# Optimization experiments

Hardware: AMD Instinct MI355X
Metric: run time of the kernel (lower is better)

The kernel has to match this reference:

```python
import jax, jax.numpy as jnp
import numpy as np

N = 100000
E = 1600000
F_IN = 512
HID = 8
HEADS = 8
NUM_CLASSES = 40
NEG_SLOPE = 0.2


def setup_inputs() -> dict:
    key = jax.random.key(0)
    ks = jax.random.split(key, 12)
    x = jax.random.normal(ks[0], (N, F_IN), dtype=jnp.float32)
    edge_index = jax.random.randint(ks[1], (2, E), 0, N, dtype=jnp.int64)
    s1 = 1.0 / np.sqrt(F_IN)
    s2 = 1.0 / np.sqrt(HID * HEADS)
    W1 = jax.random.normal(ks[2], (F_IN, HEADS * HID), dtype=jnp.float32) * s1
    a_src1 = jax.random.normal(ks[3], (HEADS, HID), dtype=jnp.float32) * s1
    a_dst1 = jax.random.normal(ks[4], (HEADS, HID), dtype=jnp.float32) * s1
    b1 = jnp.zeros((HEADS * HID,), dtype=jnp.float32)
    W2 = jax.random.normal(ks[5], (HEADS * HID, NUM_CLASSES), dtype=jnp.float32) * s2
    a_src2 = jax.random.normal(ks[6], (1, NUM_CLASSES), dtype=jnp.float32) * s2
    a_dst2 = jax.random.normal(ks[7], (1, NUM_CLASSES), dtype=jnp.float32) * s2
    b2 = jnp.zeros((NUM_CLASSES,), dtype=jnp.float32)
    return {"x": x, "edge_index": edge_index, "W1": W1, "a_src1": a_src1,
            "a_dst1": a_dst1, "b1": b1, "W2": W2, "a_src2": a_src2,
            "a_dst2": a_dst2, "b2": b2}


def _gat_conv(x, src, dst, W, a_src, a_dst, b, heads, out_ch):
    # linear projection, per-head: [N, heads, out_ch]
    h = (x @ W).reshape(N, heads, out_ch)
    # per-node attention logits [N, heads]
    al_s = jnp.einsum('nhf,hf->nh', h, a_src)
    al_d = jnp.einsum('nhf,hf->nh', h, a_dst)
    # per-edge raw scores [E', heads]
    e = jax.nn.leaky_relu(al_s[src] + al_d[dst], NEG_SLOPE)
    # segment softmax over edges sharing a destination node
    m = jax.lax.stop_gradient(jax.ops.segment_max(e, dst, num_segments=N))
    m = jnp.where(jnp.isfinite(m), m, 0.0)
    e = jnp.exp(e - m[dst])
    denom = jax.ops.segment_sum(e, dst, num_segments=N)
    alpha = e / denom[dst]  # [E', heads]
    # scatter-weighted aggregation of gathered source features
    out = jax.ops.segment_sum(alpha[:, :, None] * h[src], dst, num_segments=N)
    return out.reshape(N, heads * out_ch) + b


def reference(x, edge_index, W1, a_src1, a_dst1, b1, W2, a_src2, a_dst2, b2):
    # PyG GATConv default: add self-loops
    loops = jnp.arange(N, dtype=edge_index.dtype)
    src = jnp.concatenate([edge_index[0], loops])
    dst = jnp.concatenate([edge_index[1], loops])
    h = _gat_conv(x, src, dst, W1, a_src1, a_dst1, b1, HEADS, HID)
    h = jax.nn.elu(h)
    # dropout(p=0.6) is identity in eval mode
    out = _gat_conv(h, src, dst, W2, a_src2, a_dst2, b2, 1, NUM_CLASSES)
    return jax.nn.log_softmax(out, axis=1)
```

## Files before the change

### kernel.cpp

```cpp
#include <hip/hip_runtime.h>
#include <hip/hip_bf16.h>
#include <cstdint>
#include <cstddef>

#define N_NODES 100000
#define N_EDGES 1600000
#define E_TOT   (N_EDGES + N_NODES)
#define F_IN    512
#define HEADS   8
#define HID     8
#define F_H     64
#define NC      40
#define NEG     0.2f

#define BSH    8
#define NB     391
#define CHUNKH 8192
#define NBH    ((E_TOT + CHUNKH - 1) / CHUNKH)
#define CHUNKF 8192
#define NBF    ((E_TOT + CHUNKF - 1) / CHUNKF)
#define CAP    7168
#define GEMM_G ((N_NODES + 63) / 64)

typedef __attribute__((ext_vector_type(8))) __bf16 bf16x8;
typedef __attribute__((ext_vector_type(4))) float f32x4;
typedef __attribute__((ext_vector_type(8))) unsigned short u16x8;

__device__ __forceinline__ float bf2f(unsigned short u) {
  unsigned int w = ((unsigned int)u) << 16;
  return __builtin_bit_cast(float, w);
}
__device__ __forceinline__ unsigned short f2bf(float f) {
  __hip_bfloat16 b = __float2bfloat16(f);
  return __builtin_bit_cast(unsigned short, b);
}
__device__ __forceinline__ float lrexp(float v) {
  v = (v > 0.f) ? v : NEG * v;
  return __expf(v);
}

__device__ __forceinline__ bool detect_i64(const int* __restrict__ ei) {
  int lane = threadIdx.x & 63;
  int v = ei[2 * lane + 1];
  return __ballot(v != 0) == 0ull;
}

__device__ __forceinline__ int load_dst(const int* __restrict__ ei, bool f, int i) {
  if (i < N_EDGES) return f ? ei[2 * (N_EDGES + i)] : ei[N_EDGES + i];
  return i - N_EDGES;
}
__device__ __forceinline__ int load_src(const int* __restrict__ ei, bool f, int i) {
  if (i < N_EDGES) return f ? ei[2 * i] : ei[i];
  return i - N_EDGES;
}

__global__ __launch_bounds__(256) void k_hist_pack(
    const int* __restrict__ ei, const float* __restrict__ W1,
    uint4* __restrict__ w1f, int* __restrict__ bcnt) {
  __shared__ int h[NB];
  const int t = threadIdx.x;
  if (blockIdx.x < 16) {
    int tid = blockIdx.x * 256 + t;
    int lane = tid & 63;
    int tt = (tid >> 6) & 3;
    int s = tid >> 8;
    int k0 = s * 32 + ((lane >> 4) << 3);
    int col = tt * 16 + (lane & 15);
    u16x8 v;
#pragma unroll
    for (int i = 0; i < 8; ++i) v[i] = f2bf(W1[(size_t)(k0 + i) * F_H + col]);
    w1f[tid] = __builtin_bit_cast(uint4, v);
    return;
  }
  const int blk = blockIdx.x - 16;
  const bool f = detect_i64(ei);
  for (int i = t; i < NB; i += 256) h[i] = 0;
  __syncthreads();
  const int base = blk * CHUNKH;
#pragma unroll
  for (int j = 0; j < CHUNKH / 256; ++j) {
    int i = base + t + j * 256;
    if (i < E_TOT) atomicAdd(&h[load_dst(ei, f, i) >> BSH], 1);
  }
  __syncthreads();
  for (int i = t; i < NB; i += 256)
    if (h[i]) atomicAdd(&bcnt[i], h[i]);
}

__global__ __launch_bounds__(512) void k_bscan(const int* __restrict__ bcnt,
                                               int* __restrict__ bstart,
                                               int* __restrict__ bcur,
                                               int* __restrict__ rowstart) {
  __shared__ int sh[512];
  const int t = threadIdx.x;
  int v = (t < NB) ? bcnt[t] : 0;
  sh[t] = v;
  __syncthreads();
  for (int d = 1; d < 512; d <<= 1) {
    int u = (t >= d) ? sh[t - d] : 0;
    __syncthreads();
    sh[t] += u;
    __syncthreads();
  }
  if (t < NB) {
    int e = sh[t] - v;
    bstart[t] = e;
    bcur[t] = e;
  }
  if (t == 0) { bstart[NB] = E_TOT; rowstart[N_NODES] = E_TOT; }
}

__global__ __launch_bounds__(256) void k_bfill(const int* __restrict__ ei,
                                               int* __restrict__ bcur,
                                               unsigned int* __restrict__ inter) {
  __shared__ unsigned int ent[CHUNKF];
  __shared__ int h[NB], ofs[NB], cur[NB], gpos[NB];
  const int t = threadIdx.x;
  const int base = blockIdx.x * CHUNKF;
  const bool f = detect_i64(ei);
  for (int i = t; i < NB; i += 256) h[i] = 0;
  __syncthreads();
#pragma unroll
  for (int j = 0; j < CHUNKF / 256; ++j) {
    int i = base + t + j * 256;
    if (i < E_TOT) atomicAdd(&h[load_dst(ei, f, i) >> BSH], 1);
  }
  __syncthreads();
  if (t < 64) {
    int loc[7];
    int s = 0;
#pragma unroll
    for (int k = 0; k < 7; ++k) {
      int ix = t * 7 + k;
      int hv = (ix < NB) ? h[ix] : 0;
      loc[k] = s;
      s += hv;
    }
    int incl = s;
    for (int dd = 1; dd < 64; dd <<= 1) {
      int u = __shfl_up(incl, dd);
      if (t >= dd) incl += u;
    }
    int excl = incl - s;
#pragma unroll
    for (int k = 0; k < 7; ++k) {
      int ix = t * 7 + k;
      if (ix < NB) ofs[ix] = excl + loc[k];
    }
  }
  __syncthreads();
  for (int i = t; i < NB; i += 256) {
    cur[i] = ofs[i];
    gpos[i] = h[i] ? atomicAdd(&bcur[i], h[i]) : 0;
  }
  __syncthreads();
#pragma unroll
  for (int j = 0; j < CHUNKF / 256; ++j) {
    int i = base + t + j * 256;
    if (i < E_TOT) {
      int s = load_src(ei, f, i);
      int d = load_dst(ei, f, i);
      int p = atomicAdd(&cur[d >> BSH], 1);
      ent[p] = ((unsigned int)(d & 255) << 24) | (unsigned int)s;
    }
  }
  __syncthreads();
  const int wv = t >> 6, ln = t & 63;
  for (int b = wv; b < NB; b += 4) {
    int c = h[b];
    if (!c) continue;
    int g = gpos[b], o = ofs[b];
    for (int i = ln; i < c; i += 64) inter[g + i] = ent[o + i];
  }
}

__global__ __launch_bounds__(256) void k_gemm1s(
    const float* __restrict__ x, const uint4* __restrict__ w1f,
    const float* __restrict__ a_src, const float* __restrict__ a_dst,
    unsigned short* __restrict__ h1b, float* __restrict__ als,
    float* __restrict__ ald) {
  constexpr int PITCH = 68;
  __shared__ float xs[64 * PITCH];
  const int t = threadIdx.x;
  const int lane = t & 63;
  const int wv = t >> 6;
  const int rb = blockIdx.x * 64;
  const int srow = t >> 4;
  const int scol = t & 15;
  const int myrow = wv * 16 + (lane & 15);
  const int koff = (lane >> 4) << 3;

  f32x4 acc[4];
#pragma unroll
  for (int i = 0; i < 4; ++i) acc[i] = (f32x4){0.f, 0.f, 0.f, 0.f};

  for (int kc = 0; kc < F_IN; kc += 64) {
    __syncthreads();
#pragma unroll
    for (int j = 0; j < 4; ++j) {
      int r = srow + j * 16;
      int gr = rb + r;
      float4 v = make_float4(0.f, 0.f, 0.f, 0.f);
      if (gr < N_NODES)
        v = *reinterpret_cast<const float4*>(&x[(size_t)gr * F_IN + kc + scol * 4]);
      *reinterpret_cast<float4*>(&xs[r * PITCH + scol * 4]) = v;
    }
    __syncthreads();
#pragma unroll
    for (int s2 = 0; s2 < 2; ++s2) {
      const int sg = (kc >> 5) + s2;
      float4 a0 = *reinterpret_cast<const float4*>(&xs[myrow * PITCH + s2 * 32 + koff]);
      float4 a1 = *reinterpret_cast<const float4*>(&xs[myrow * PITCH + s2 * 32 + koff + 4]);
      uint4 b0 = w1f[(sg * 4 + 0) * 64 + lane];
      uint4 b1 = w1f[(sg * 4 + 1) * 64 + lane];
      uint4 b2 = w1f[(sg * 4 + 2) * 64 + lane];
      uint4 b3 = w1f[(sg * 4 + 3) * 64 + lane];
      bf16x8 af;
      af[0] = (__bf16)a0.x; af[1] = (__bf16)a0.y;
      af[2] = (__bf16)a0.z; af[3] = (__bf16)a0.w;
      af[4] = (__bf16)a1.x; af[5] = (__bf16)a1.y;
      af[6] = (__bf16)a1.z; af[7] = (__bf16)a1.w;
      acc[0] = __builtin_amdgcn_mfma_f32_16x16x32_bf16(af, __builtin_bit_cast(bf16x8, b0), acc[0], 0, 0, 0);
      acc[1] = __builtin_amdgcn_mfma_f32_16x16x32_bf16(af, __builtin_bit_cast(bf16x8, b1), acc[1], 0, 0, 0);
      acc[2] = __builtin_amdgcn_mfma_f32_16x16x32_bf16(af, __builtin_bit_cast(bf16x8, b2), acc[2], 0, 0, 0);
      acc[3] = __builtin_amdgcn_mfma_f32_16x16x32_bf16(af, __builtin_bit_cast(bf16x8, b3), acc[3], 0, 0, 0);
    }
  }

  const int r0 = rb + wv * 16 + ((lane >> 4) << 2);
  const int c = lane & 15;
#pragma unroll
  for (int tt = 0; tt < 4; ++tt) {
#pragma unroll
    for (int i = 0; i < 4; ++i) {
      int r = r0 + i;
      if (r < N_NODES) h1b[(size_t)r * F_H + tt * 16 + c] = f2bf(acc[tt][i]);
    }
  }

  float asw[4], adw[4];
#pragma unroll
  for (int tt = 0; tt < 4; ++tt) {
    asw[tt] = a_src[tt * 16 + c];
    adw[tt] = a_dst[tt * 16 + c];
  }
  float sp[4][4], dp[4][4];
#pragma unroll
  for (int tt = 0; tt < 4; ++tt)
#pragma unroll
    for (int i = 0; i < 4; ++i) {
      sp[tt][i] = acc[tt][i] * asw[tt];
      dp[tt][i] = acc[tt][i] * adw[tt];
    }
#pragma unroll
  for (int dd = 1; dd < 8; dd <<= 1)
#pragma unroll
    for (int tt = 0; tt < 4; ++tt)
#pragma unroll
      for (int i = 0; i < 4; ++i) {
        sp[tt][i] += __shfl_xor(sp[tt][i], dd);
        dp[tt][i] += __shfl_xor(dp[tt][i], dd);
      }
  if ((c & 7) == 0) {
    const int hb = c >> 3;
#pragma unroll
    for (int i = 0; i < 4; ++i) {
      int r = r0 + i;
      if (r < N_NODES) {
#pragma unroll
        for (int tt = 0; tt < 4; ++tt) {
          als[(size_t)r * HEADS + tt * 2 + hb] = sp[tt][i];
          ald[(size_t)r * HEADS + tt * 2 + hb] = dp[tt][i];
        }
      }
    }
  }
}

__global__ __launch_bounds__(256) void k_cfill(const unsigned int* __restrict__ inter,
                                               const int* __restrict__ bstart,
                                               int* __restrict__ rowstart,
                                               int* __restrict__ csrc) {
  __shared__ unsigned int out_l[CAP];
  __shared__ int cnt[256], sc[256], cur2[256];
  const int t = threadIdx.x;
  const int b = blockIdx.x;
  const int segStart = bstart[b];
  const int L = bstart[b + 1] - segStart;
  cnt[t] = 0;
  __syncthreads();
  for (int i = t; i < L; i += 256) atomicAdd(&cnt[inter[segStart + i] >> 24], 1);
  __syncthreads();
  sc[t] = cnt[t];
  __syncthreads();
  for (int d = 1; d < 256; d <<= 1) {
    int v = (t >= d) ? sc[t - d] : 0;
    __syncthreads();
    sc[t] += v;
    __syncthreads();
  }
  const int excl = sc[t] - cnt[t];
  cur2[t] = excl;
  const int node = (b << BSH) + t;
  if (node < N_NODES) rowstart[node] = segStart + excl;
  __syncthreads();
  if (L <= CAP) {
    for (int i = t; i < L; i += 256) {
      unsigned int e = inter[segStart + i];
      int p = atomicAdd(&cur2[e >> 24], 1);
      out_l[p] = e & 0xFFFFFFu;
    }
    __syncthreads();
    for (int i = t; i < L; i += 256) csrc[segStart + i] = (int)out_l[i];
  } else {
    for (int i = t; i < L; i += 256) {
      unsigned int e = inter[segStart + i];
      int p = atomicAdd(&cur2[e >> 24], 1);
      csrc[segStart + p] = (int)(e & 0xFFFFFFu);
    }
  }
}

__global__ __launch_bounds__(256) void k_agg1n(
    const int* __restrict__ rowstart, const int* __restrict__ csrc,
    const unsigned short* __restrict__ h1b, const float* __restrict__ als,
    const float* __restrict__ ald, const float* __restrict__ b1,
    unsigned short* __restrict__ hactb) {
  const int w = (int)((blockIdx.x * 256 + threadIdx.x) >> 6);
  const int lane = threadIdx.x & 63;
  const int grp = lane >> 3;
  const int l = lane & 7;
  const int n = w * 8 + grp;
  const bool live = (n < N_NODES);
  const int e0 = live ? rowstart[n] : 0;
  const int e1 = live ? rowstart[n + 1] : 0;
  const float aldv = live ? ald[(size_t)n * HEADS + l] : 0.f;

  float den = 0.f;
  float acc[8];
#pragma unroll
  for (int k = 0; k < 8; ++k) acc[k] = 0.f;

  int e = e0;
  for (; e + 4 <= e1; e += 4) {
    int4 sv = *reinterpret_cast<const int4*>(&csrc[e]);
    float a0 = als[(size_t)sv.x * HEADS + l];
    float a1 = als[(size_t)sv.y * HEADS + l];
    float a2 = als[(size_t)sv.z * HEADS + l];
    float a3 = als[(size_t)sv.w * HEADS + l];
    uint4 u0 = *reinterpret_cast<const uint4*>(&h1b[(size_t)sv.x * F_H + l * 8]);
    uint4 u1 = *reinterpret_cast<const uint4*>(&h1b[(size_t)sv.y * F_H + l * 8]);
    uint4 u2 = *reinterpret_cast<const uint4*>(&h1b[(size_t)sv.z * F_H + l * 8]);
    uint4 u3 = *reinterpret_cast<const uint4*>(&h1b[(size_t)sv.w * F_H + l * 8]);
    float p0 = lrexp(a0 + aldv), p1 = lrexp(a1 + aldv);
    float p2 = lrexp(a2 + aldv), p3 = lrexp(a3 + aldv);
    den += (p0 + p1) + (p2 + p3);
    const unsigned int* q0 = &u0.x;
    const unsigned int* q1 = &u1.x;
    const unsigned int* q2 = &u2.x;
    const unsigned int* q3 = &u3.x;
#pragma unroll
    for (int k = 0; k < 4; ++k) {
      acc[2 * k]     += p0 * bf2f((unsigned short)q0[k]) + p1 * bf2f((unsigned short)q1[k])
                      + p2 * bf2f((unsigned short)q2[k]) + p3 * bf2f((unsigned short)q3[k]);
      acc[2 * k + 1] += p0 * bf2f((unsigned short)(q0[k] >> 16)) + p1 * bf2f((unsigned short)(q1[k] >> 16))
                      + p2 * bf2f((unsigned short)(q2[k] >> 16)) + p3 * bf2f((unsigned short)(q3[k] >> 16));
    }
  }
  for (; e < e1; ++e) {
    int s = csrc[e];
    float a = als[(size_t)s * HEADS + l];
    uint4 u = *reinterpret_cast<const uint4*>(&h1b[(size_t)s * F_H + l * 8]);
    float p = lrexp(a + aldv);
    den += p;
    const unsigned int* q = &u.x;
#pragma unroll
    for (int k = 0; k < 4; ++k) {
      acc[2 * k]     += p * bf2f((unsigned short)q[k]);
      acc[2 * k + 1] += p * bf2f((unsigned short)(q[k] >> 16));
    }
  }

  if (live) {
    float inv = 1.f / den;
    uint4 outw;
    unsigned int* ow = &outw.x;
#pragma unroll
    for (int k = 0; k < 4; ++k) {
      float ox = acc[2 * k] * inv + b1[l * 8 + 2 * k];
      float oy = acc[2 * k + 1] * inv + b1[l * 8 + 2 * k + 1];
      ox = (ox > 0.f) ? ox : expm1f(ox);
      oy = (oy > 0.f) ? oy : expm1f(oy);
      ow[k] = ((unsigned int)f2bf(oy) << 16) | (unsigned int)f2bf(ox);
    }
    *reinterpret_cast<uint4*>(&hactb[(size_t)n * F_H + l * 8]) = outw;
  }
}

__global__ __launch_bounds__(256) void k_l2proj(
    const unsigned short* __restrict__ hactb, const float* __restrict__ W2,
    const float* __restrict__ a_src2, const float* __restrict__ a_dst2,
    unsigned short* __restrict__ h2b, float* __restrict__ als2,
    float* __restrict__ ald2) {
  __shared__ float hs[64 * 68];
  __shared__ float w2s[F_H * NC];
  const int t = threadIdx.x;
  const int nb = blockIdx.x * 64;
  {
    int r0 = t >> 3, c8 = t & 7;
#pragma unroll
    for (int i = 0; i < 2; ++i) {
      int r = r0 + i * 32;
      int gr = nb + r;
      u16x8 v = (u16x8)(0);
      if (gr < N_NODES)
        v = *reinterpret_cast<const u16x8*>(&hactb[(size_t)gr * F_H + c8 * 8]);
#pragma unroll
      for (int k = 0; k < 8; ++k) hs[r * 68 + c8 * 8 + k] = bf2f(v[k]);
    }
  }
  for (int i = t; i < F_H * NC; i += 256) w2s[i] = W2[i];
  __syncthreads();

  const int node = t >> 2, cg = t & 3;
  float acc[10];
#pragma unroll
  for (int c = 0; c < 10; ++c) acc[c] = 0.f;
  for (int k = 0; k < F_H; ++k) {
    float xv = hs[node * 68 + k];
#pragma unroll
    for (int c = 0; c < 10; ++c) acc[c] += xv * w2s[k * NC + cg * 10 + c];
  }
  const int gn = nb + node;
  float ps = 0.f, pd = 0.f;
#pragma unroll
  for (int c = 0; c < 10; ++c) {
    ps += acc[c] * a_src2[cg * 10 + c];
    pd += acc[c] * a_dst2[cg * 10 + c];
  }
  ps += __shfl_xor(ps, 1); ps += __shfl_xor(ps, 2);
  pd += __shfl_xor(pd, 1); pd += __shfl_xor(pd, 2);
  if (gn < N_NODES) {
#pragma unroll
    for (int c = 0; c < 10; ++c) h2b[(size_t)gn * NC + cg * 10 + c] = f2bf(acc[c]);
    if (cg == 0) { als2[gn] = ps; ald2[gn] = pd; }
  }
}

__global__ __launch_bounds__(256) void k_agg2n(
    const int* __restrict__ rowstart, const int* __restrict__ csrc,
    const unsigned short* __restrict__ h2b, const float* __restrict__ als2,
    const float* __restrict__ ald2, const float* __restrict__ b2,
    float* __restrict__ out) {
  const int w = (int)((blockIdx.x * 256 + threadIdx.x) >> 6);
  const int lane = threadIdx.x & 63;
  const int grp = lane >> 3;
  const int l = lane & 7;
  const int n = w * 8 + grp;
  const bool live = (n < N_NODES);
  const int e0 = live ? rowstart[n] : 0;
  const int e1 = live ? rowstart[n + 1] : 0;
  const float aldv = live ? ald2[n] : 0.f;
  const bool act = (l < 5);
  const int fo = act ? l * 8 : 0;

  float den = 0.f;
  float acc[8];
#pragma unroll
  for (int k = 0; k < 8; ++k) acc[k] = 0.f;

  int e = e0;
  for (; e + 4 <= e1; e += 4) {
    int4 sv = *reinterpret_cast<const int4*>(&csrc[e]);
    float a0 = als2[sv.x], a1 = als2[sv.y], a2 = als2[sv.z], a3 = als2[sv.w];
    uint4 u0 = *reinterpret_cast<const uint4*>(&h2b[(size_t)sv.x * NC + fo]);
    uint4 u1 = *reinterpret_cast<const uint4*>(&h2b[(size_t)sv.y * NC + fo]);
    uint4 u2 = *reinterpret_cast<const uint4*>(&h2b[(size_t)sv.z * NC + fo]);
    uint4 u3 = *reinterpret_cast<const uint4*>(&h2b[(size_t)sv.w * NC + fo]);
    float p0 = lrexp(a0 + aldv), p1 = lrexp(a1 + aldv);
    float p2 = lrexp(a2 + aldv), p3 = lrexp(a3 + aldv);
    den += (p0 + p1) + (p2 + p3);
    const unsigned int* q0 = &u0.x;
    const unsigned int* q1 = &u1.x;
    const unsigned int* q2 = &u2.x;
    const unsigned int* q3 = &u3.x;
#pragma unroll
    for (int k = 0; k < 4; ++k) {
      acc[2 * k]     += p0 * bf2f((unsigned short)q0[k]) + p1 * bf2f((unsigned short)q1[k])
                      + p2 * bf2f((unsigned short)q2[k]) + p3 * bf2f((unsigned short)q3[k]);
      acc[2 * k + 1] += p0 * bf2f((unsigned short)(q0[k] >> 16)) + p1 * bf2f((unsigned short)(q1[k] >> 16))
                      + p2 * bf2f((unsigned short)(q2[k] >> 16)) + p3 * bf2f((unsigned short)(q3[k] >> 16));
    }
  }
  for (; e < e1; ++e) {
    int s = csrc[e];
    float a = als2[s];
    uint4 u = *reinterpret_cast<const uint4*>(&h2b[(size_t)s * NC + fo]);
    float p = lrexp(a + aldv);
    den += p;
    const unsigned int* q = &u.x;
#pragma unroll
    for (int k = 0; k < 4; ++k) {
      acc[2 * k]     += p * bf2f((unsigned short)q[k]);
      acc[2 * k + 1] += p * bf2f((unsigned short)(q[k] >> 16));
    }
  }

  float o[8];
  float inv = 1.f / den;
  float mx = -1e30f;
#pragma unroll
  for (int k = 0; k < 8; ++k) {
    o[k] = act ? (acc[k] * inv + b2[fo + k]) : -1e30f;
    mx = fmaxf(mx, o[k]);
  }
  mx = fmaxf(mx, __shfl_xor(mx, 1));
  mx = fmaxf(mx, __shfl_xor(mx, 2));
  mx = fmaxf(mx, __shfl_xor(mx, 4));
  float se = 0.f;
#pragma unroll
  for (int k = 0; k < 8; ++k) se += act ? __expf(o[k] - mx) : 0.f;
  se += __shfl_xor(se, 1);
  se += __shfl_xor(se, 2);
  se += __shfl_xor(se, 4);
  if (live && act) {
    float ls = __logf(se);
    float4 r0, r1;
    r0.x = o[0] - mx - ls; r0.y = o[1] - mx - ls;
    r0.z = o[2] - mx - ls; r0.w = o[3] - mx - ls;
    r1.x = o[4] - mx - ls; r1.y = o[5] - mx - ls;
    r1.z = o[6] - mx - ls; r1.w = o[7] - mx - ls;
    *reinterpret_cast<float4*>(&out[(size_t)n * NC + l * 8]) = r0;
    *reinterpret_cast<float4*>(&out[(size_t)n * NC + l * 8 + 4]) = r1;
  }
}

extern "C" void kernel_launch(void* const* d_in, const int* in_sizes, int n_in,
                              void* d_out, int out_size, void* d_ws, size_t ws_size,
                              hipStream_t stream) {
  const float* x      = (const float*)d_in[0];
  const int*   ei     = (const int*)d_in[1];
  const float* W1     = (const float*)d_in[2];
  const float* a_src1 = (const float*)d_in[3];
  const float* a_dst1 = (const float*)d_in[4];
  const float* b1     = (const float*)d_in[5];
  const float* W2     = (const float*)d_in[6];
  const float* a_src2 = (const float*)d_in[7];
  const float* a_dst2 = (const float*)d_in[8];
  const float* b2     = (const float*)d_in[9];
  float* out = (float*)d_out;

  char* ws = (char*)d_ws;
  size_t o = 0;
  auto carve = [&](size_t bytes) -> char* {
    char* p = ws + o;
    o = (o + bytes + 255) & ~(size_t)255;
    return p;
  };
  int*   bcnt     = (int*)carve((size_t)NB * 4);
  int*   bstart   = (int*)carve((size_t)(NB + 1) * 4);
  int*   bcur     = (int*)carve((size_t)NB * 4);
  int*   rowstart = (int*)carve((size_t)(N_NODES + 1) * 4);
  unsigned int* inter = (unsigned int*)carve((size_t)E_TOT * 4);
  int*   csrc     = (int*)carve((size_t)(E_TOT + 8) * 4);
  uint4* w1f      = (uint4*)carve((size_t)4096 * 16);
  unsigned short* h1b   = (unsigned short*)carve((size_t)N_NODES * F_H * 2);
  float* als1     = (float*)carve((size_t)N_NODES * HEADS * 4);
  float* ald1     = (float*)carve((size_t)N_NODES * HEADS * 4);
  unsigned short* hactb = (unsigned short*)carve((size_t)N_NODES * F_H * 2);
  unsigned short* h2b   = (unsigned short*)carve((size_t)(N_NODES * NC + 8) * 2);
  float* als2     = (float*)carve((size_t)N_NODES * 4);
  float* ald2     = (float*)carve((size_t)N_NODES * 4);
  (void)ws_size; (void)n_in; (void)in_sizes; (void)out_size;

  hipMemsetAsync(bcnt, 0, (size_t)NB * 4, stream);
  k_hist_pack<<<16 + NBH, 256, 0, stream>>>(ei, W1, w1f, bcnt);
  k_bscan<<<1, 512, 0, stream>>>(bcnt, bstart, bcur, rowstart);
  k_bfill<<<NBF, 256, 0, stream>>>(ei, bcur, inter);
  k_gemm1s<<<GEMM_G, 256, 0, stream>>>(x, w1f, a_src1, a_dst1, h1b, als1, ald1);
  k_cfill<<<NB, 256, 0, stream>>>(inter, bstart, rowstart, csrc);

  const int aggGrid = (N_NODES + 31) / 32;
  k_agg1n<<<aggGrid, 256, 0, stream>>>(rowstart, csrc, h1b, als1, ald1, b1, hactb);
  k_l2proj<<<(N_NODES + 63) / 64, 256, 0, stream>>>(hactb, W2, a_src2, a_dst2, h2b, als2, ald2);
  k_agg2n<<<aggGrid, 256, 0, stream>>>(rowstart, csrc, h2b, als2, ald2, b2, out);
}
```

Before: 271.3 us.

## Double-buffer GEMM1 x tiles with direct global-to-LDS loads and XOR swizzle

After: 255.3 us. -5.9%, faster.

```diff
diff --git a/kernel.cpp b/kernel.cpp
--- a/kernel.cpp
+++ b/kernel.cpp
@@ -174,43 +174,58 @@
   }
 }
 
-__global__ __launch_bounds__(256) void k_gemm1s(
+__global__ __launch_bounds__(256) void k_gemm1g(
     const float* __restrict__ x, const uint4* __restrict__ w1f,
     const float* __restrict__ a_src, const float* __restrict__ a_dst,
     unsigned short* __restrict__ h1b, float* __restrict__ als,
     float* __restrict__ ald) {
-  constexpr int PITCH = 68;
-  __shared__ float xs[64 * PITCH];
+  __shared__ float xs[2 * 64 * 64];
   const int t = threadIdx.x;
   const int lane = t & 63;
   const int wv = t >> 6;
   const int rb = blockIdx.x * 64;
-  const int srow = t >> 4;
-  const int scol = t & 15;
+
+  const int srow_in_kb = lane >> 4;
+  const int sc16 = lane & 15;
+
   const int myrow = wv * 16 + (lane & 15);
-  const int koff = (lane >> 4) << 3;
+  const int m7 = myrow & 7;
+  const int rowbase = myrow * 64;
+  const int cg2 = (lane >> 4) << 1;
 
   f32x4 acc[4];
 #pragma unroll
   for (int i = 0; i < 4; ++i) acc[i] = (f32x4){0.f, 0.f, 0.f, 0.f};
 
-  for (int kc = 0; kc < F_IN; kc += 64) {
-    __syncthreads();
+  auto STAGE = [&](int buf, int p) {
 #pragma unroll
     for (int j = 0; j < 4; ++j) {
-      int r = srow + j * 16;
+      int kb = wv * 4 + j;
+      int r = kb * 4 + srow_in_kb;
       int gr = rb + r;
-      float4 v = make_float4(0.f, 0.f, 0.f, 0.f);
-      if (gr < N_NODES)
-        v = *reinterpret_cast<const float4*>(&x[(size_t)gr * F_IN + kc + scol * 4]);
-      *reinterpret_cast<float4*>(&xs[r * PITCH + scol * 4]) = v;
-    }
-    __syncthreads();
+      if (gr >= N_NODES) gr = N_NODES - 1;
+      int c16s = sc16 ^ (r & 7);
+      const float* src = x + (size_t)gr * F_IN + p * 64 + c16s * 4;
+      char* dst = (char*)xs + buf * 16384 + kb * 1024;
+      __builtin_amdgcn_global_load_lds(
+          (const __attribute__((address_space(1))) void*)src,
+          (__attribute__((address_space(3))) void*)dst, 16, 0, 0);
+    }
+  };
+
+  STAGE(0, 0);
+  __syncthreads();
+  int buf = 0;
+#pragma unroll
+  for (int p = 0; p < 8; ++p) {
+    if (p < 7) STAGE(buf ^ 1, p + 1);
+    const float* bufp = xs + buf * 4096;
 #pragma unroll
     for (int s2 = 0; s2 < 2; ++s2) {
-      const int sg = (kc >> 5) + s2;
-      float4 a0 = *reinterpret_cast<const float4*>(&xs[myrow * PITCH + s2 * 32 + koff]);
-      float4 a1 = *reinterpret_cast<const float4*>(&xs[myrow * PITCH + s2 * 32 + koff + 4]);
+      const int sg = p * 2 + s2;
+      const int c16a = s2 * 8 + cg2;
+      float4 a0 = *reinterpret_cast<const float4*>(&bufp[rowbase + ((c16a ^ m7) << 2)]);
+      float4 a1 = *reinterpret_cast<const float4*>(&bufp[rowbase + (((c16a + 1) ^ m7) << 2)]);
       uint4 b0 = w1f[(sg * 4 + 0) * 64 + lane];
       uint4 b1 = w1f[(sg * 4 + 1) * 64 + lane];
       uint4 b2 = w1f[(sg * 4 + 2) * 64 + lane];
@@ -225,6 +240,8 @@
       acc[2] = __builtin_amdgcn_mfma_f32_16x16x32_bf16(af, __builtin_bit_cast(bf16x8, b2), acc[2], 0, 0, 0);
       acc[3] = __builtin_amdgcn_mfma_f32_16x16x32_bf16(af, __builtin_bit_cast(bf16x8, b3), acc[3], 0, 0, 0);
     }
+    __syncthreads();
+    buf ^= 1;
   }
 
   const int r0 = rb + wv * 16 + ((lane >> 4) << 2);
@@ -577,7 +594,7 @@
   k_hist_pack<<<16 + NBH, 256, 0, stream>>>(ei, W1, w1f, bcnt);
   k_bscan<<<1, 512, 0, stream>>>(bcnt, bstart, bcur, rowstart);
   k_bfill<<<NBF, 256, 0, stream>>>(ei, bcur, inter);
-  k_gemm1s<<<GEMM_G, 256, 0, stream>>>(x, w1f, a_src1, a_dst1, h1b, als1, ald1);
+  k_gemm1g<<<GEMM_G, 256, 0, stream>>>(x, w1f, a_src1, a_dst1, h1b, als1, ald1);
   k_cfill<<<NB, 256, 0, stream>>>(inter, bstart, rowstart, csrc);
 
   const int aggGrid = (N_NODES + 31) / 32;
```
